# Kernel optimization log

Measured on AMD Instinct MI355X. Metric: run time of the kernel, lower is better.

The kernel has to match this reference:

```python
import jax, jax.numpy as jnp
import numpy as np

DIM = 768
H = 12
HD = 64  # head_dim = dim // num_heads
SCALE = HD ** (-0.5)
EPS = 1e-6


def setup_inputs() -> dict:
    key = jax.random.key(0)
    k1, k2, k3, k4, k5 = jax.random.split(key, 5)
    B, N = 8, 1024
    x = jax.random.normal(k1, (B, N, DIM), dtype=jnp.float32)
    policy = jax.random.uniform(k2, (B, N, 1), dtype=jnp.float32)
    # nn.Linear weights: [out_features, in_features]; qkv_bias=False, proj has bias
    qkv_w = jax.random.normal(k3, (3 * H * HD, DIM), dtype=jnp.float32) * (DIM ** -0.5)
    proj_w = jax.random.normal(k4, (DIM, H * HD), dtype=jnp.float32) * ((H * HD) ** -0.5)
    proj_b = jax.random.normal(k5, (DIM,), dtype=jnp.float32) * 0.01
    return {"x": x, "policy": policy, "qkv_w": qkv_w, "proj_w": proj_w, "proj_b": proj_b}


def _softmax_with_policy(attn, policy):
    # attn: [B,H,N,N], policy: [B,N,1]
    B, Hh, N, _ = attn.shape
    attn_policy = policy.reshape(B, 1, 1, N)
    eye = jnp.eye(N, dtype=attn_policy.dtype).reshape(1, 1, N, N)
    attn_policy = attn_policy + (1.0 - attn_policy) * eye
    max_att = jnp.max(attn, axis=-1, keepdims=True)
    a = jnp.exp((attn - max_att).astype(jnp.float32)) * attn_policy.astype(jnp.float32)
    a = (a + EPS / N) / (jnp.sum(a, axis=-1, keepdims=True) + EPS)
    return a.astype(max_att.dtype)


def reference(x, policy, qkv_w, proj_w, proj_b):
    B, N, C = x.shape
    qkv = (x @ qkv_w.T).reshape(B, N, 3, H, HD)
    qkv = jnp.transpose(qkv, (2, 0, 3, 1, 4))  # [3,B,H,N,HD]
    q, k, v = qkv[0], qkv[1], qkv[2]
    attn = jnp.einsum('bhnd,bhmd->bhnm', q * SCALE, k)  # [B,H,N,N]
    attn = _softmax_with_policy(attn, policy)
    out = jnp.einsum('bhnm,bhmd->bhnd', attn, v)  # [B,H,N,HD]
    out = jnp.transpose(out, (0, 2, 1, 3)).reshape(B, N, H * HD)
    return out @ proj_w.T + proj_b
```

## Files before the change

### kernel.cpp

```cpp
#include <hip/hip_runtime.h>

typedef __bf16 bf16x8 __attribute__((ext_vector_type(8)));
typedef float floatx4 __attribute__((ext_vector_type(4)));

#define EPSF 1e-6f

__device__ inline unsigned short f2bf(float f) {
  union { float f; unsigned u; } x; x.f = f;
  unsigned r = x.u + 0x7FFFu + ((x.u >> 16) & 1u);
  return (unsigned short)(r >> 16);
}
__device__ inline float bf2f(unsigned short u) {
  union { unsigned u; float f; } x; x.u = ((unsigned)u) << 16;
  return x.f;
}
__device__ inline unsigned pk2bf(float lo, float hi) {
  union { float f; unsigned u; } a, b; a.f = lo; b.f = hi;
  unsigned ua = a.u + 0x8000u, ub = b.u + 0x8000u;
  return (ub & 0xFFFF0000u) | (ua >> 16);
}
__device__ inline float fexp2(float x) { return __builtin_amdgcn_exp2f(x); }

__device__ inline floatx4 mfma16(bf16x8 a, bf16x8 b, floatx4 c) {
  return __builtin_amdgcn_mfma_f32_16x16x32_bf16(a, b, c, 0, 0, 0);
}

__device__ inline void gll16(const unsigned short* g, unsigned short* l) {
  __builtin_amdgcn_global_load_lds((__attribute__((address_space(1))) void*)g,
                                   (__attribute__((address_space(3))) void*)l, 16, 0, 0);
}

__device__ __host__ inline int sigma_inv(int p) {
  const int qq = p >> 3, jj = p & 7;
  return (jj < 4) ? (qq * 4 + jj) : (16 + qq * 4 + jj - 4);
}

__global__ __launch_bounds__(256) void prep_kernel(const float* __restrict__ x,
                                                   const float* __restrict__ qkv_w,
                                                   const float* __restrict__ proj_w,
                                                   const float* __restrict__ policy,
                                                   unsigned short* __restrict__ xb,
                                                   unsigned short* __restrict__ wqkv,
                                                   unsigned short* __restrict__ wproj,
                                                   unsigned short* __restrict__ pbf) {
  const int bid = blockIdx.x, tid = threadIdx.x;
  if (bid < 3072) {
    const int i = bid * 2048 + tid * 8;
    float4 v0 = *(const float4*)(x + i);
    float4 v1 = *(const float4*)(x + i + 4);
    __align__(16) unsigned short o[8] = {f2bf(v0.x), f2bf(v0.y), f2bf(v0.z), f2bf(v0.w),
                                         f2bf(v1.x), f2bf(v1.y), f2bf(v1.z), f2bf(v1.w)};
    *(float4*)(xb + i) = *(float4*)o;
  } else if (bid < 3936) {
    const int i = (bid - 3072) * 2048 + tid * 8;
    const float s = (i < 589824) ? 0.18033688011112042f : 1.0f;
    float4 v0 = *(const float4*)(qkv_w + i);
    float4 v1 = *(const float4*)(qkv_w + i + 4);
    __align__(16) unsigned short o[8] = {
        f2bf(v0.x * s), f2bf(v0.y * s), f2bf(v0.z * s), f2bf(v0.w * s),
        f2bf(v1.x * s), f2bf(v1.y * s), f2bf(v1.z * s), f2bf(v1.w * s)};
    *(float4*)(wqkv + i) = *(float4*)o;
  } else if (bid < 4224) {
    const int i0 = (bid - 3936) * 2048 + tid * 8;
    const int base = (i0 / 768) * 768 + ((i0 % 768) & ~63);
    __align__(16) unsigned short o[8];
#pragma unroll
    for (int t = 0; t < 8; t++) {
      const int cp = (i0 + t) & 63;
      const int c = 16 * (cp & 3) + (cp >> 2);
      o[t] = f2bf(proj_w[base + c]);
    }
    *(float4*)(wproj + i0) = *(float4*)o;
  } else {
    const int idx = (bid - 4224) * 256 + tid;
    const int b = idx >> 10, g = idx & 1023;
    const int c = ((g >> 5) << 5) + sigma_inv(g & 31);
    pbf[idx] = f2bf(policy[b * 1024 + c]);
  }
}

template <int EP, int BN, int W>
__global__ __launch_bounds__(256, W) void gemm_bt(const unsigned short* __restrict__ A,
                                                  const unsigned short* __restrict__ Bt,
                                                  void* __restrict__ Cout,
                                                  const float* __restrict__ bias,
                                                  int M, int N, int K) {
  constexpr int J = BN / 32;
  __shared__ __align__(16) unsigned short sA[128 * 64];
  __shared__ __align__(16) unsigned short sB[BN * 64];
  const int bid = blockIdx.x;
  const int yb = (bid & 7) * 8 + ((bid >> 3) & 7);
  const int xb_ = bid >> 6;
  const int m0 = yb * 128, n0 = xb_ * BN;
  const int tid = threadIdx.x;
  const int lane = tid & 63, wave = tid >> 6;
  const int qd = lane >> 4, l15 = lane & 15;
  const int wr = (wave >> 1) * 64, wc = (wave & 1) * (BN / 2);
  const int srow = tid >> 3;
  const int scb = (tid & 7) ^ (srow & 7);
  const unsigned short* Ag = A + (long)(m0 + srow) * K + scb * 8;
  const unsigned short* Bg = Bt + (long)(n0 + srow) * K + scb * 8;
  const int x7 = l15 & 7;
  floatx4 acc[4][J] = {};
  for (int k0 = 0; k0 < K; k0 += 64) {
    __syncthreads();
#pragma unroll
    for (int p = 0; p < 4; p++) gll16(Ag + (long)(p * 32) * K + k0, sA + p * 2048 + wave * 512);
#pragma unroll
    for (int p = 0; p < J; p++) gll16(Bg + (long)(p * 32) * K + k0, sB + p * 2048 + wave * 512);
    __syncthreads();
#pragma unroll
    for (int s = 0; s < 2; s++) {
      const int cw = ((s * 4 + qd) ^ x7) * 8;
      bf16x8 af[4], bf[J];
#pragma unroll
      for (int i = 0; i < 4; i++) af[i] = *(const bf16x8*)&sA[(wr + i * 16 + l15) * 64 + cw];
#pragma unroll
      for (int j = 0; j < J; j++) bf[j] = *(const bf16x8*)&sB[(wc + j * 16 + l15) * 64 + cw];
#pragma unroll
      for (int i = 0; i < 4; i++)
#pragma unroll
        for (int j = 0; j < J; j++) acc[i][j] = mfma16(af[i], bf[j], acc[i][j]);
    }
  }
  if constexpr (EP == 0) {
#pragma unroll
    for (int i = 0; i < 4; i++)
#pragma unroll
      for (int r = 0; r < 4; r++) {
        const int row = m0 + wr + i * 16 + qd * 4 + r;
        __align__(8) unsigned short pk[4];
#pragma unroll
        for (int j = 0; j < 4; j++) pk[j] = f2bf(acc[i][j][r]);
        *(uint2*)((unsigned short*)Cout + (long)row * N + n0 + wc + 4 * l15) = *(uint2*)pk;
      }
  } else {
#pragma unroll
    for (int i = 0; i < 4; i++)
#pragma unroll
      for (int j = 0; j < J; j++) {
        const int col = n0 + wc + j * 16 + l15;
#pragma unroll
        for (int r = 0; r < 4; r++) {
          const int row = m0 + wr + i * 16 + qd * 4 + r;
          ((float*)Cout)[(long)row * N + col] = acc[i][j][r] + bias[col];
        }
      }
  }
}

__global__ __launch_bounds__(256) void transpose_v(const unsigned short* __restrict__ qkv,
                                                   const float* __restrict__ policy,
                                                   unsigned short* __restrict__ vTp) {
  __shared__ unsigned short tile[64][72];
  __shared__ float sPol[64];
  const int bh = blockIdx.y;
  const int b = bh / 12, h = bh % 12;
  const int n0 = blockIdx.x * 64;
  const int t = threadIdx.x;
  if (t < 64) sPol[t] = policy[b * 1024 + n0 + t];
  {
    const int nr = t >> 2, dc = (t & 3) * 16;
    const unsigned short* src = qkv + (long)(b * 1024 + n0 + nr) * 2304 + 2 * 768 + h * 64 + dc;
    float4 v0 = *(const float4*)src;
    float4 v1 = *(const float4*)(src + 8);
    *(float4*)&tile[nr][dc] = v0;
    *(float4*)&tile[nr][dc + 8] = v1;
  }
  __syncthreads();
  {
    const int d = t >> 2, nc = (t & 3) * 16;
    __align__(16) unsigned short o[16];
#pragma unroll
    for (int jj = 0; jj < 16; jj++) {
      const int cc = nc + jj;
      const int cl = (cc & 32) + sigma_inv(cc & 31);
      o[jj] = f2bf(bf2f(tile[cl][d]) * sPol[cl]);
    }
    unsigned short* dst = vTp + (long)(bh * 64 + d) * 1024 + n0 + nc;
    *(float4*)dst = *(float4*)&o[0];
    *(float4*)(dst + 8) = *(float4*)&o[8];
  }
}

__global__ __launch_bounds__(256, 3) void attn_kernel(const unsigned short* __restrict__ qkv,
                                                      const unsigned short* __restrict__ vTp,
                                                      const unsigned short* __restrict__ pbf,
                                                      const float* __restrict__ policy,
                                                      unsigned short* __restrict__ aout) {
  __shared__ __align__(16) unsigned short sK[4][2048];
  __shared__ __align__(16) unsigned short sV[4][2048];
  __shared__ __align__(16) unsigned short sPv[1024];
  __shared__ float sD[4][32];
  const int bid = blockIdx.x;
  const int bh = bid % 96, qt = bid / 96;
  const int b = bh / 12, h = bh % 12;
  const int tid = threadIdx.x;
  const int wave = tid >> 6, lane = tid & 63;
  const int qd = lane >> 4, l15 = lane & 15;
  const int q0 = qt * 128 + wave * 32;
  const unsigned short* qb = qkv + (long)(b * 1024 + q0 + l15) * 2304 + h * 64 + qd * 8;
  bf16x8 qf00 = *(const bf16x8*)qb;
  bf16x8 qf01 = *(const bf16x8*)(qb + 32);
  bf16x8 qf10 = *(const bf16x8*)(qb + (long)16 * 2304);
  bf16x8 qf11 = *(const bf16x8*)(qb + (long)16 * 2304 + 32);
  if (tid < 128) *(float4*)(sPv + tid * 8) = *(const float4*)(pbf + b * 1024 + tid * 8);
  const int krow = wave * 8 + (lane >> 3);
  const int kcb = (lane & 7) ^ (lane >> 3);
  const unsigned short* kgl = qkv + (long)(b * 1024 + krow) * 2304 + 768 + h * 64 + kcb * 8;
  const int vrow = tid >> 2;
  const int vcb = (tid & 3) ^ ((vrow ^ (vrow >> 2)) & 3);
  const unsigned short* vgl = vTp + (long)(bh * 64 + vrow) * 1024 + vcb * 8;
  const int x7 = l15 & 7;
  const int vsw = (qd ^ ((l15 ^ (l15 >> 2)) & 3)) * 8;
  floatx4 O0[4] = {}, O1[4] = {};
  floatx4 Dl0 = {}, Dl1 = {};
  const floatx4 z = {0.f, 0.f, 0.f, 0.f};
#pragma unroll
  for (int c = 0; c < 3; ++c) {
    gll16(kgl + (long)(32 * c) * 2304, &sK[c][wave * 512]);
    gll16(vgl + 32 * c, &sV[c][wave * 512]);
  }
  asm volatile("s_waitcnt vmcnt(2) lgkmcnt(0)" ::: "memory");
  __builtin_amdgcn_s_barrier();
  asm volatile("" ::: "memory");
  bf16x8 kf00 = *(const bf16x8*)&sK[0][(0 + l15) * 64 + ((0 + qd) ^ x7) * 8];
  bf16x8 kf01 = *(const bf16x8*)&sK[0][(0 + l15) * 64 + ((4 + qd) ^ x7) * 8];
  bf16x8 kf10 = *(const bf16x8*)&sK[0][(16 + l15) * 64 + ((0 + qd) ^ x7) * 8];
  bf16x8 kf11 = *(const bf16x8*)&sK[0][(16 + l15) * 64 + ((4 + qd) ^ x7) * 8];
  for (int it = 0; it < 32; ++it) {
    const int buf = it & 3;
    if (it < 29) {
      const long co = (long)(32 * (it + 3));
      gll16(kgl + co * 2304, &sK[(it + 3) & 3][wave * 512]);
      gll16(vgl + co, &sV[(it + 3) & 3][wave * 512]);
    }
    const int c0 = it * 32;
    bf16x8 pv = *(const bf16x8*)&sPv[c0 + qd * 8];
    __builtin_amdgcn_s_setprio(1);
    floatx4 tA0 = mfma16(kf01, qf01, mfma16(kf00, qf00, z));
    floatx4 tB0 = mfma16(kf11, qf01, mfma16(kf10, qf00, z));
    floatx4 tA1 = mfma16(kf01, qf11, mfma16(kf00, qf10, z));
    floatx4 tB1 = mfma16(kf11, qf11, mfma16(kf10, qf10, z));
    __builtin_amdgcn_s_setprio(0);
    const int nb = (it + 1) & 3;
    bf16x8 nk00 = *(const bf16x8*)&sK[nb][(0 + l15) * 64 + ((0 + qd) ^ x7) * 8];
    bf16x8 nk01 = *(const bf16x8*)&sK[nb][(0 + l15) * 64 + ((4 + qd) ^ x7) * 8];
    bf16x8 nk10 = *(const bf16x8*)&sK[nb][(16 + l15) * 64 + ((0 + qd) ^ x7) * 8];
    bf16x8 nk11 = *(const bf16x8*)&sK[nb][(16 + l15) * 64 + ((4 + qd) ^ x7) * 8];
    uint4 pu0, pu1;
    pu0.x = pk2bf(fexp2(tA0[0]), fexp2(tA0[1]));
    pu0.y = pk2bf(fexp2(tA0[2]), fexp2(tA0[3]));
    pu0.z = pk2bf(fexp2(tB0[0]), fexp2(tB0[1]));
    pu0.w = pk2bf(fexp2(tB0[2]), fexp2(tB0[3]));
    pu1.x = pk2bf(fexp2(tA1[0]), fexp2(tA1[1]));
    pu1.y = pk2bf(fexp2(tA1[2]), fexp2(tA1[3]));
    pu1.z = pk2bf(fexp2(tB1[0]), fexp2(tB1[1]));
    pu1.w = pk2bf(fexp2(tB1[2]), fexp2(tB1[3]));
    bf16x8 pf0 = *(bf16x8*)&pu0;
    bf16x8 pf1 = *(bf16x8*)&pu1;
    bf16x8 vf0 = *(const bf16x8*)&sV[buf][(0 * 16 + l15) * 32 + vsw];
    bf16x8 vf1 = *(const bf16x8*)&sV[buf][(1 * 16 + l15) * 32 + vsw];
    bf16x8 vf2 = *(const bf16x8*)&sV[buf][(2 * 16 + l15) * 32 + vsw];
    bf16x8 vf3 = *(const bf16x8*)&sV[buf][(3 * 16 + l15) * 32 + vsw];
    __builtin_amdgcn_s_setprio(1);
    Dl0 = mfma16(pf0, pv, Dl0);
    Dl1 = mfma16(pf1, pv, Dl1);
    O0[0] = mfma16(pf0, vf0, O0[0]); O1[0] = mfma16(pf1, vf0, O1[0]);
    O0[1] = mfma16(pf0, vf1, O0[1]); O1[1] = mfma16(pf1, vf1, O1[1]);
    O0[2] = mfma16(pf0, vf2, O0[2]); O1[2] = mfma16(pf1, vf2, O1[2]);
    O0[3] = mfma16(pf0, vf3, O0[3]); O1[3] = mfma16(pf1, vf3, O1[3]);
    __builtin_amdgcn_s_setprio(0);
    kf00 = nk00; kf01 = nk01; kf10 = nk10; kf11 = nk11;
    if (it < 29) asm volatile("s_waitcnt vmcnt(2)" ::: "memory");
    else         asm volatile("s_waitcnt vmcnt(0)" ::: "memory");
    __builtin_amdgcn_s_barrier();
    asm volatile("" ::: "memory");
  }
  {
    const unsigned short* kd = qkv + (long)(b * 1024 + q0 + l15) * 2304 + 768 + h * 64 + qd * 8;
    bf16x8 kd00 = *(const bf16x8*)kd;
    bf16x8 kd01 = *(const bf16x8*)(kd + 32);
    bf16x8 kd10 = *(const bf16x8*)(kd + (long)16 * 2304);
    bf16x8 kd11 = *(const bf16x8*)(kd + (long)16 * 2304 + 32);
    float part0 = 0.f, part1 = 0.f;
#pragma unroll
    for (int jj = 0; jj < 8; jj++) {
      part0 += (float)qf00[jj] * (float)kd00[jj] + (float)qf01[jj] * (float)kd01[jj];
      part1 += (float)qf10[jj] * (float)kd10[jj] + (float)qf11[jj] * (float)kd11[jj];
    }
    part0 += __shfl_xor(part0, 16); part0 += __shfl_xor(part0, 32);
    part1 += __shfl_xor(part1, 16); part1 += __shfl_xor(part1, 32);
    const float p0 = policy[b * 1024 + q0 + l15];
    const float p1 = policy[b * 1024 + q0 + 16 + l15];
    if (qd == 0) {
      sD[wave][l15] = fexp2(part0) * (1.0f - p0);
      sD[wave][16 + l15] = fexp2(part1) * (1.0f - p1);
    }
    __builtin_amdgcn_s_waitcnt(0);
    const unsigned short* vdiag = qkv + (long)(b * 1024 + q0) * 2304 + 1536 + h * 64 + l15;
#pragma unroll
    for (int r = 0; r < 4; r++) {
      const int row = qd * 4 + r;
      const float c0v = sD[wave][row], c1v = sD[wave][16 + row];
#pragma unroll
      for (int j = 0; j < 4; j++) {
        O0[j][r] += c0v * bf2f(vdiag[(long)row * 2304 + j * 16]);
        O1[j][r] += c1v * bf2f(vdiag[(long)(16 + row) * 2304 + j * 16]);
      }
      Dl0[r] += c0v;
      Dl1[r] += c1v;
    }
  }
  const long ob = (long)(b * 1024 + q0 + qd * 4) * 768 + h * 64 + l15;
#pragma unroll
  for (int r = 0; r < 4; r++) {
    const float li0 = 1.0f / (Dl0[r] + EPSF);
    const float li1 = 1.0f / (Dl1[r] + EPSF);
#pragma unroll
    for (int j = 0; j < 4; j++) {
      aout[ob + (long)r * 768 + j * 16] = f2bf(O0[j][r] * li0);
      aout[ob + (long)(16 * 768) + r * 768 + j * 16] = f2bf(O1[j][r] * li1);
    }
  }
}

extern "C" void kernel_launch(void* const* d_in, const int* in_sizes, int n_in,
                              void* d_out, int out_size, void* d_ws, size_t ws_size,
                              hipStream_t stream) {
  const float* x      = (const float*)d_in[0];
  const float* policy = (const float*)d_in[1];
  const float* qkv_w  = (const float*)d_in[2];
  const float* proj_w = (const float*)d_in[3];
  const float* proj_b = (const float*)d_in[4];
  float* out = (float*)d_out;

  char* ws = (char*)d_ws;
  unsigned short* xb    = (unsigned short*)(ws + 0);
  unsigned short* wqkv  = (unsigned short*)(ws + 12582912);
  unsigned short* wproj = (unsigned short*)(ws + 16121856);
  unsigned short* qkvb  = (unsigned short*)(ws + 17301504);
  unsigned short* vTp   = (unsigned short*)(ws + 55050240);
  unsigned short* aoutb = (unsigned short*)(ws + 67633152);
  unsigned short* pbf   = (unsigned short*)(ws + 80216064);

  prep_kernel<<<4256, 256, 0, stream>>>(x, qkv_w, proj_w, policy, xb, wqkv, wproj, pbf);
  gemm_bt<0, 128, 4><<<dim3(18 * 64), 256, 0, stream>>>(xb, wqkv, qkvb, nullptr, 8192, 2304, 768);
  transpose_v<<<dim3(16, 96), 256, 0, stream>>>(qkvb, policy, vTp);
  attn_kernel<<<dim3(768), 256, 0, stream>>>(qkvb, vTp, pbf, policy, aoutb);
  gemm_bt<1, 64, 3><<<dim3(12 * 64), 256, 0, stream>>>(aoutb, wproj, out, proj_b, 8192, 768, 768);
}
```

Baseline: 178.9 us.

## Use two waves per attention block with 64 query rows each

Restructures the attention kernel from four waves handling 32 query rows each to two waves handling 64 rows each, so every K/V fragment read from shared memory feeds twice as many MFMAs. Each thread now issues two global-to-LDS loads per K and V chunk to fill the same tile with half the threads. The cost is more accumulator registers per wave (16 output tiles), fewer waves per block, and lower occupancy bounds, which could reduce latency hiding.

```diff
diff --git a/kernel.cpp b/kernel.cpp
--- a/kernel.cpp
+++ b/kernel.cpp
@@ -183,7 +183,7 @@
   }
 }
 
-__global__ __launch_bounds__(256, 3) void attn_kernel(const unsigned short* __restrict__ qkv,
+__global__ __launch_bounds__(128, 2) void attn_kernel(const unsigned short* __restrict__ qkv,
                                                       const unsigned short* __restrict__ vTp,
                                                       const unsigned short* __restrict__ pbf,
                                                       const float* __restrict__ policy,
@@ -191,20 +191,22 @@
   __shared__ __align__(16) unsigned short sK[4][2048];
   __shared__ __align__(16) unsigned short sV[4][2048];
   __shared__ __align__(16) unsigned short sPv[1024];
-  __shared__ float sD[4][32];
+  __shared__ float sD[2][64];
   const int bid = blockIdx.x;
   const int bh = bid % 96, qt = bid / 96;
   const int b = bh / 12, h = bh % 12;
   const int tid = threadIdx.x;
   const int wave = tid >> 6, lane = tid & 63;
   const int qd = lane >> 4, l15 = lane & 15;
-  const int q0 = qt * 128 + wave * 32;
+  const int q0 = qt * 128 + wave * 64;
   const unsigned short* qb = qkv + (long)(b * 1024 + q0 + l15) * 2304 + h * 64 + qd * 8;
-  bf16x8 qf00 = *(const bf16x8*)qb;
-  bf16x8 qf01 = *(const bf16x8*)(qb + 32);
-  bf16x8 qf10 = *(const bf16x8*)(qb + (long)16 * 2304);
-  bf16x8 qf11 = *(const bf16x8*)(qb + (long)16 * 2304 + 32);
-  if (tid < 128) *(float4*)(sPv + tid * 8) = *(const float4*)(pbf + b * 1024 + tid * 8);
+  bf16x8 qf[4][2];
+#pragma unroll
+  for (int m = 0; m < 4; m++) {
+    qf[m][0] = *(const bf16x8*)(qb + (long)(m * 16) * 2304);
+    qf[m][1] = *(const bf16x8*)(qb + (long)(m * 16) * 2304 + 32);
+  }
+  *(float4*)(sPv + tid * 8) = *(const float4*)(pbf + b * 1024 + tid * 8);
   const int krow = wave * 8 + (lane >> 3);
   const int kcb = (lane & 7) ^ (lane >> 3);
   const unsigned short* kgl = qkv + (long)(b * 1024 + krow) * 2304 + 768 + h * 64 + kcb * 8;
@@ -213,15 +215,17 @@
   const unsigned short* vgl = vTp + (long)(bh * 64 + vrow) * 1024 + vcb * 8;
   const int x7 = l15 & 7;
   const int vsw = (qd ^ ((l15 ^ (l15 >> 2)) & 3)) * 8;
-  floatx4 O0[4] = {}, O1[4] = {};
-  floatx4 Dl0 = {}, Dl1 = {};
+  floatx4 O[4][4] = {};
+  floatx4 Dl[4] = {};
   const floatx4 z = {0.f, 0.f, 0.f, 0.f};
 #pragma unroll
   for (int c = 0; c < 3; ++c) {
     gll16(kgl + (long)(32 * c) * 2304, &sK[c][wave * 512]);
+    gll16(kgl + (long)(32 * c + 16) * 2304, &sK[c][1024 + wave * 512]);
     gll16(vgl + 32 * c, &sV[c][wave * 512]);
-  }
-  asm volatile("s_waitcnt vmcnt(2) lgkmcnt(0)" ::: "memory");
+    gll16(vgl + (long)32 * 1024 + 32 * c, &sV[c][1024 + wave * 512]);
+  }
+  asm volatile("s_waitcnt vmcnt(4) lgkmcnt(0)" ::: "memory");
   __builtin_amdgcn_s_barrier();
   asm volatile("" ::: "memory");
   bf16x8 kf00 = *(const bf16x8*)&sK[0][(0 + l15) * 64 + ((0 + qd) ^ x7) * 8];
@@ -232,95 +236,88 @@
     const int buf = it & 3;
     if (it < 29) {
       const long co = (long)(32 * (it + 3));
-      gll16(kgl + co * 2304, &sK[(it + 3) & 3][wave * 512]);
-      gll16(vgl + co, &sV[(it + 3) & 3][wave * 512]);
+      const int nb3 = (it + 3) & 3;
+      gll16(kgl + co * 2304, &sK[nb3][wave * 512]);
+      gll16(kgl + (co + 16) * 2304, &sK[nb3][1024 + wave * 512]);
+      gll16(vgl + co, &sV[nb3][wave * 512]);
+      gll16(vgl + (long)32 * 1024 + co, &sV[nb3][1024 + wave * 512]);
     }
     const int c0 = it * 32;
     bf16x8 pv = *(const bf16x8*)&sPv[c0 + qd * 8];
+    floatx4 tA[4], tB[4];
     __builtin_amdgcn_s_setprio(1);
-    floatx4 tA0 = mfma16(kf01, qf01, mfma16(kf00, qf00, z));
-    floatx4 tB0 = mfma16(kf11, qf01, mfma16(kf10, qf00, z));
-    floatx4 tA1 = mfma16(kf01, qf11, mfma16(kf00, qf10, z));
-    floatx4 tB1 = mfma16(kf11, qf11, mfma16(kf10, qf10, z));
+#pragma unroll
+    for (int m = 0; m < 4; m++) {
+      tA[m] = mfma16(kf01, qf[m][1], mfma16(kf00, qf[m][0], z));
+      tB[m] = mfma16(kf11, qf[m][1], mfma16(kf10, qf[m][0], z));
+    }
     __builtin_amdgcn_s_setprio(0);
     const int nb = (it + 1) & 3;
     bf16x8 nk00 = *(const bf16x8*)&sK[nb][(0 + l15) * 64 + ((0 + qd) ^ x7) * 8];
     bf16x8 nk01 = *(const bf16x8*)&sK[nb][(0 + l15) * 64 + ((4 + qd) ^ x7) * 8];
     bf16x8 nk10 = *(const bf16x8*)&sK[nb][(16 + l15) * 64 + ((0 + qd) ^ x7) * 8];
     bf16x8 nk11 = *(const bf16x8*)&sK[nb][(16 + l15) * 64 + ((4 + qd) ^ x7) * 8];
-    uint4 pu0, pu1;
-    pu0.x = pk2bf(fexp2(tA0[0]), fexp2(tA0[1]));
-    pu0.y = pk2bf(fexp2(tA0[2]), fexp2(tA0[3]));
-    pu0.z = pk2bf(fexp2(tB0[0]), fexp2(tB0[1]));
-    pu0.w = pk2bf(fexp2(tB0[2]), fexp2(tB0[3]));
-    pu1.x = pk2bf(fexp2(tA1[0]), fexp2(tA1[1]));
-    pu1.y = pk2bf(fexp2(tA1[2]), fexp2(tA1[3]));
-    pu1.z = pk2bf(fexp2(tB1[0]), fexp2(tB1[1]));
-    pu1.w = pk2bf(fexp2(tB1[2]), fexp2(tB1[3]));
-    bf16x8 pf0 = *(bf16x8*)&pu0;
-    bf16x8 pf1 = *(bf16x8*)&pu1;
     bf16x8 vf0 = *(const bf16x8*)&sV[buf][(0 * 16 + l15) * 32 + vsw];
     bf16x8 vf1 = *(const bf16x8*)&sV[buf][(1 * 16 + l15) * 32 + vsw];
     bf16x8 vf2 = *(const bf16x8*)&sV[buf][(2 * 16 + l15) * 32 + vsw];
     bf16x8 vf3 = *(const bf16x8*)&sV[buf][(3 * 16 + l15) * 32 + vsw];
-    __builtin_amdgcn_s_setprio(1);
-    Dl0 = mfma16(pf0, pv, Dl0);
-    Dl1 = mfma16(pf1, pv, Dl1);
-    O0[0] = mfma16(pf0, vf0, O0[0]); O1[0] = mfma16(pf1, vf0, O1[0]);
-    O0[1] = mfma16(pf0, vf1, O0[1]); O1[1] = mfma16(pf1, vf1, O1[1]);
-    O0[2] = mfma16(pf0, vf2, O0[2]); O1[2] = mfma16(pf1, vf2, O1[2]);
-    O0[3] = mfma16(pf0, vf3, O0[3]); O1[3] = mfma16(pf1, vf3, O1[3]);
-    __builtin_amdgcn_s_setprio(0);
+#pragma unroll
+    for (int m = 0; m < 4; m++) {
+      uint4 pu;
+      pu.x = pk2bf(fexp2(tA[m][0]), fexp2(tA[m][1]));
+      pu.y = pk2bf(fexp2(tA[m][2]), fexp2(tA[m][3]));
+      pu.z = pk2bf(fexp2(tB[m][0]), fexp2(tB[m][1]));
+      pu.w = pk2bf(fexp2(tB[m][2]), fexp2(tB[m][3]));
+      bf16x8 pf = *(bf16x8*)&pu;
+      Dl[m] = mfma16(pf, pv, Dl[m]);
+      O[m][0] = mfma16(pf, vf0, O[m][0]);
+      O[m][1] = mfma16(pf, vf1, O[m][1]);
+      O[m][2] = mfma16(pf, vf2, O[m][2]);
+      O[m][3] = mfma16(pf, vf3, O[m][3]);
+    }
     kf00 = nk00; kf01 = nk01; kf10 = nk10; kf11 = nk11;
-    if (it < 29) asm volatile("s_waitcnt vmcnt(2)" ::: "memory");
+    if (it < 29) asm volatile("s_waitcnt vmcnt(4)" ::: "memory");
     else         asm volatile("s_waitcnt vmcnt(0)" ::: "memory");
     __builtin_amdgcn_s_barrier();
     asm volatile("" ::: "memory");
   }
   {
-    const unsigned short* kd = qkv + (long)(b * 1024 + q0 + l15) * 2304 + 768 + h * 64 + qd * 8;
-    bf16x8 kd00 = *(const bf16x8*)kd;
-    bf16x8 kd01 = *(const bf16x8*)(kd + 32);
-    bf16x8 kd10 = *(const bf16x8*)(kd + (long)16 * 2304);
-    bf16x8 kd11 = *(const bf16x8*)(kd + (long)16 * 2304 + 32);
-    float part0 = 0.f, part1 = 0.f;
-#pragma unroll
-    for (int jj = 0; jj < 8; jj++) {
-      part0 += (float)qf00[jj] * (float)kd00[jj] + (float)qf01[jj] * (float)kd01[jj];
-      part1 += (float)qf10[jj] * (float)kd10[jj] + (float)qf11[jj] * (float)kd11[jj];
-    }
-    part0 += __shfl_xor(part0, 16); part0 += __shfl_xor(part0, 32);
-    part1 += __shfl_xor(part1, 16); part1 += __shfl_xor(part1, 32);
-    const float p0 = policy[b * 1024 + q0 + l15];
-    const float p1 = policy[b * 1024 + q0 + 16 + l15];
-    if (qd == 0) {
-      sD[wave][l15] = fexp2(part0) * (1.0f - p0);
-      sD[wave][16 + l15] = fexp2(part1) * (1.0f - p1);
+#pragma unroll
+    for (int m = 0; m < 4; m++) {
+      const unsigned short* kd =
+          qkv + (long)(b * 1024 + q0 + m * 16 + l15) * 2304 + 768 + h * 64 + qd * 8;
+      bf16x8 kd0 = *(const bf16x8*)kd;
+      bf16x8 kd1 = *(const bf16x8*)(kd + 32);
+      float pt = 0.f;
+#pragma unroll
+      for (int jj = 0; jj < 8; jj++)
+        pt += (float)qf[m][0][jj] * (float)kd0[jj] + (float)qf[m][1][jj] * (float)kd1[jj];
+      pt += __shfl_xor(pt, 16);
+      pt += __shfl_xor(pt, 32);
+      const float pm = policy[b * 1024 + q0 + m * 16 + l15];
+      if (qd == 0) sD[wave][m * 16 + l15] = fexp2(pt) * (1.0f - pm);
     }
     __builtin_amdgcn_s_waitcnt(0);
     const unsigned short* vdiag = qkv + (long)(b * 1024 + q0) * 2304 + 1536 + h * 64 + l15;
 #pragma unroll
+    for (int m = 0; m < 4; m++)
+#pragma unroll
+      for (int r = 0; r < 4; r++) {
+        const int row = m * 16 + qd * 4 + r;
+        const float cv = sD[wave][row];
+#pragma unroll
+        for (int j = 0; j < 4; j++) O[m][j][r] += cv * bf2f(vdiag[(long)row * 2304 + j * 16]);
+        Dl[m][r] += cv;
+      }
+  }
+#pragma unroll
+  for (int m = 0; m < 4; m++) {
+    const long ob = (long)(b * 1024 + q0 + m * 16 + qd * 4) * 768 + h * 64 + l15;
+#pragma unroll
     for (int r = 0; r < 4; r++) {
-      const int row = qd * 4 + r;
-      const float c0v = sD[wave][row], c1v = sD[wave][16 + row];
-#pragma unroll
-      for (int j = 0; j < 4; j++) {
-        O0[j][r] += c0v * bf2f(vdiag[(long)row * 2304 + j * 16]);
-        O1[j][r] += c1v * bf2f(vdiag[(long)(16 + row) * 2304 + j * 16]);
-      }
-      Dl0[r] += c0v;
-      Dl1[r] += c1v;
-    }
-  }
-  const long ob = (long)(b * 1024 + q0 + qd * 4) * 768 + h * 64 + l15;
-#pragma unroll
-  for (int r = 0; r < 4; r++) {
-    const float li0 = 1.0f / (Dl0[r] + EPSF);
-    const float li1 = 1.0f / (Dl1[r] + EPSF);
-#pragma unroll
-    for (int j = 0; j < 4; j++) {
-      aout[ob + (long)r * 768 + j * 16] = f2bf(O0[j][r] * li0);
-      aout[ob + (long)(16 * 768) + r * 768 + j * 16] = f2bf(O1[j][r] * li1);
+      const float li = 1.0f / (Dl[m][r] + EPSF);
+#pragma unroll
+      for (int j = 0; j < 4; j++) aout[ob + (long)r * 768 + j * 16] = f2bf(O[m][j][r] * li);
     }
   }
 }
@@ -347,6 +344,6 @@
   prep_kernel<<<4256, 256, 0, stream>>>(x, qkv_w, proj_w, policy, xb, wqkv, wproj, pbf);
   gemm_bt<0, 128, 4><<<dim3(18 * 64), 256, 0, stream>>>(xb, wqkv, qkvb, nullptr, 8192, 2304, 768);
   transpose_v<<<dim3(16, 96), 256, 0, stream>>>(qkvb, policy, vTp);
-  attn_kernel<<<dim3(768), 256, 0, stream>>>(qkvb, vTp, pbf, policy, aoutb);
+  attn_kernel<<<dim3(768), 128, 0, stream>>>(qkvb, vTp, pbf, policy, aoutb);
   gemm_bt<1, 64, 3><<<dim3(12 * 64), 256, 0, stream>>>(aoutb, wproj, out, proj_b, 8192, 768, 768);
 }
```

Result: slower. 182.5 us (+2.0%).
